# Optimization experiments

Measured on AMD Instinct MI355X. Metric: run time of the kernel, lower is better.

Reference implementation:

```python
import jax, jax.numpy as jnp
import numpy as np

B, N, M, D = 64, 512, 512, 2
BLUR, SCALING, DIAMETER, P = 0.01, 0.9, 4.0, 2


def _eps_schedule():
    # geomloss epsilon_schedule: geometric decay of temperature eps = sigma^p
    # from diameter^p down to blur^p with ratio scaling^p.
    e = np.arange(P * np.log(DIAMETER), P * np.log(BLUR), P * np.log(SCALING))
    return np.concatenate([[DIAMETER ** P], np.exp(e), [BLUR ** P]]).astype(np.float32)


def setup_inputs() -> dict:
    key = jax.random.key(0)
    k1, k2, k3, k4, k5 = jax.random.split(key, 5)
    a = jax.random.uniform(k1, (B, N), dtype=jnp.float32)
    a = a / a.sum(-1, keepdims=True)  # probability weights of measure 1
    b = jax.random.uniform(k2, (B, M), dtype=jnp.float32)
    b = b / b.sum(-1, keepdims=True)  # probability weights of measure 2
    x = jax.random.normal(k3, (B, N, D), dtype=jnp.float32)
    y = jax.random.normal(k4, (B, M, D), dtype=jnp.float32)
    w = jax.random.uniform(k5, (B,), dtype=jnp.float32)  # per-sample weights
    return {"prob1": a, "coord1": x, "prob2": b, "coord2": y, "weights": w}


def _softmin(eps, C, h):
    # softmin_eps(C, h)_i = -eps * log sum_j exp(h_j - C_ij / eps)
    # C: [B,N,M], h: [B,M] -> [B,N]
    return -eps * jax.nn.logsumexp(h[:, None, :] - C / eps, axis=2)


def reference(prob1, coord1, prob2, coord2, weights):
    a, x, b, y = prob1, coord1, prob2, coord2
    # p=2 cost: C(x,y) = |x-y|^2 / 2 (geomloss convention)
    C_xy = 0.5 * jnp.sum((x[:, :, None, :] - y[:, None, :, :]) ** 2, axis=-1)  # [B,N,M]
    C_yx = jnp.swapaxes(C_xy, 1, 2)  # [B,M,N]
    a_log = jnp.log(a)
    b_log = jnp.log(b)

    eps_arr = jnp.asarray(_eps_schedule())
    eps0 = eps_arr[0]
    # initialization at the coarsest temperature
    f = _softmin(eps0, C_xy, b_log)  # [B,N] dual potential on x
    g = _softmin(eps0, C_yx, a_log)  # [B,M] dual potential on y

    def step(carry, eps):
        f, g = carry
        ft = _softmin(eps, C_xy, b_log + g / eps)
        gt = _softmin(eps, C_yx, a_log + f / eps)
        return (0.5 * (f + ft), 0.5 * (g + gt)), None

    (f, g), _ = jax.lax.scan(step, (f, g), eps_arr)

    # geomloss runs the loop without grad and does one last extrapolation step
    f = jax.lax.stop_gradient(f)
    g = jax.lax.stop_gradient(g)
    eps_last = jnp.float32(BLUR ** P)
    f_fin = _softmin(eps_last, C_xy, b_log + g / eps_last)
    g_fin = _softmin(eps_last, C_yx, a_log + f / eps_last)

    # OT_eps(a, b) = <a, f> + <b, g>  (debias=False)
    batch_loss = jnp.sum(a * f_fin, axis=-1) + jnp.sum(b * g_fin, axis=-1)  # [B]
    return jnp.sum(batch_loss * weights)
```

## Files before the change

kernel.cpp:

```cpp
#include <hip/hip_runtime.h>
#include <cmath>

#define B_ 64
#define NP 512

constexpr float L2E  = 1.4426950408889634f;
constexpr float LN2f = 0.6931471805599453f;

struct EpsList { float e[64]; };

__device__ __forceinline__ float exp2_fast(float v) {
#if __has_builtin(__builtin_amdgcn_exp2f)
    return __builtin_amdgcn_exp2f(v);
#else
    return exp2f(v);
#endif
}
__device__ __forceinline__ float log2_fast(float v) {
#if __has_builtin(__builtin_amdgcn_logf)
    return __builtin_amdgcn_logf(v);
#else
    return log2f(v);
#endif
}

__global__ __launch_bounds__(256, 2) void sinkhorn_coop(
    const float* __restrict__ a, const float* __restrict__ x,
    const float* __restrict__ bb, const float* __restrict__ y,
    float* __restrict__ fA, float* __restrict__ gA,
    float* __restrict__ fB, float* __restrict__ gB,
    unsigned int* __restrict__ bar, float* __restrict__ part2,
    EpsList el, int n_eps)
{
    __shared__ float4 sreg[NP];
    __shared__ float4 sd[NP];
    __shared__ float s_eps[64];
    __shared__ float swred[4];

    const int bid = blockIdx.x;
    const int b   = bid >> 3;
    const int q   = bid & 7;
    const bool gside = q >= 4;
    const int rq  = q & 3;
    const int tid = threadIdx.x;
    const int oct = tid & 7;
    const int rowbase = rq * 128 + (tid >> 3) * 4;
    unsigned int* own_ctr  = bar + b * 64 + (gside ? 32 : 0);
    unsigned int* othr_ctr = bar + b * 64 + (gside ? 0 : 32);

    if (tid < 64) s_eps[tid] = el.e[tid];

    const float2* oc2   = (const float2*)(gside ? (x + b * NP * 2) : (y + b * NP * 2));
    const float*  oprob = gside ? (a + b * NP) : (bb + b * NP);
    #pragma unroll
    for (int u2 = 0; u2 < 2; ++u2) {
        int t = tid + u2 * 256;
        float2 c = oc2[t];
        sreg[t] = make_float4(c.x, c.y, fmaf(c.y, c.y, c.x * c.x),
                              L2E * logf(oprob[t]));
    }
    const float* mcoord = gside ? (y + b * NP * 2) : (x + b * NP * 2);
    const float* mprob  = gside ? (bb + b * NP)    : (a + b * NP);
    const float4 rc01 = *(const float4*)(mcoord + rowbase * 2);
    const float4 rc23 = *(const float4*)(mcoord + rowbase * 2 + 4);
    float x0[4] = {rc01.x, rc01.z, rc23.x, rc23.z};
    float x1[4] = {rc01.y, rc01.w, rc23.y, rc23.w};
    float half_n2[4];
    #pragma unroll
    for (int r = 0; r < 4; ++r) half_n2[r] = 0.5f * fmaf(x1[r], x1[r], x0[r] * x0[r]);

    float pv[4];
    const int n_pass = n_eps + 2;
    __syncthreads();

    for (int p = 0; p < n_pass; ++p) {
        const float eps = (p == 0) ? s_eps[0]
                        : (p <= n_eps ? s_eps[p - 1] : s_eps[n_eps - 1]);
        const float inv_eps = 1.0f / eps;
        const float ieL2E = inv_eps * L2E;
        const float nie   = -0.5f * ieL2E;

        float* opot = (gside ? ((p & 1) ? fA : fB)
                             : ((p & 1) ? gA : gB)) + b * NP;
        #pragma unroll
        for (int u2 = 0; u2 < 2; ++u2) {
            int t = tid + u2 * 256;
            float4 sr = sreg[t];
            float pot = (p != 0)
                ? __hip_atomic_load(opot + t, __ATOMIC_RELAXED, __HIP_MEMORY_SCOPE_AGENT)
                : 0.0f;
            float h2 = fmaf(pot, ieL2E, sr.w);
            sd[t] = make_float4(sr.x, sr.y, fmaf(nie, sr.z, h2), 0.0f);
        }
        __syncthreads();

        float x0p[4], x1p[4], m[4], s[4];
        #pragma unroll
        for (int r = 0; r < 4; ++r) {
            x0p[r] = x0[r] * ieL2E;
            x1p[r] = x1[r] * ieL2E;
            m[r] = -INFINITY;
            s[r] = 0.0f;
        }

        #pragma unroll 1
        for (int k = 0; k < 8; ++k) {
            float4 cj[8];
            #pragma unroll
            for (int u2 = 0; u2 < 8; ++u2) cj[u2] = sd[64 * k + 8 * u2 + oct];
            #pragma unroll
            for (int r = 0; r < 4; ++r) {
                float arg[8];
                #pragma unroll
                for (int u2 = 0; u2 < 8; ++u2)
                    arg[u2] = fmaf(x1p[r], cj[u2].y, fmaf(x0p[r], cj[u2].x, cj[u2].z));
                float cm = fmaxf(fmaxf(fmaxf(arg[0], arg[1]), fmaxf(arg[2], arg[3])),
                                 fmaxf(fmaxf(arg[4], arg[5]), fmaxf(arg[6], arg[7])));
                float mn = fmaxf(m[r], cm);
                s[r] *= exp2_fast(m[r] - mn);
                #pragma unroll
                for (int u2 = 0; u2 < 8; ++u2) s[r] += exp2_fast(arg[u2] - mn);
                m[r] = mn;
            }
        }

        float val[4];
        #pragma unroll
        for (int r = 0; r < 4; ++r) {
            float mr = m[r], sr = s[r];
            #pragma unroll
            for (int d = 1; d <= 4; d <<= 1) {
                float mo = __shfl_xor(mr, d);
                float so = __shfl_xor(sr, d);
                float mt = fmaxf(mr, mo);
                sr = sr * exp2_fast(mr - mt) + so * exp2_fast(mo - mt);
                mr = mt;
            }
            val[r] = fmaf(-eps * LN2f, mr + log2_fast(sr), half_n2[r]);
        }

        if (p >= 1 && p <= n_eps) {
            #pragma unroll
            for (int r = 0; r < 4; ++r) val[r] = 0.5f * (pv[r] + val[r]);
        }
        #pragma unroll
        for (int r = 0; r < 4; ++r) pv[r] = val[r];

        if (p == n_pass - 1) break;

        if (oct == 0) {
            float* dst = (gside ? ((p & 1) ? gB : gA)
                                : ((p & 1) ? fB : fA)) + b * NP + rowbase;
            #pragma unroll
            for (int r = 0; r < 4; ++r)
                __hip_atomic_store(dst + r, val[r], __ATOMIC_RELAXED,
                                   __HIP_MEMORY_SCOPE_AGENT);
        }

        __syncthreads();
        if (tid == 0) {
            __hip_atomic_fetch_add(own_ctr, 1u, __ATOMIC_RELAXED,
                                   __HIP_MEMORY_SCOPE_AGENT);
            const unsigned int target = 4u * (unsigned int)(p + 1);
            unsigned int guard = 0;
            while (__hip_atomic_load(othr_ctr, __ATOMIC_RELAXED,
                                     __HIP_MEMORY_SCOPE_AGENT) < target) {
                __builtin_amdgcn_s_sleep(1);
                if (++guard > (1u << 20)) break;
            }
        }
        __syncthreads();
    }

    float local = 0.0f;
    if (oct == 0) {
        const float4 pr = *(const float4*)(mprob + rowbase);
        local = pr.x * pv[0] + pr.y * pv[1] + pr.z * pv[2] + pr.w * pv[3];
    }
    #pragma unroll
    for (int o = 32; o > 0; o >>= 1) local += __shfl_down(local, o);
    if ((tid & 63) == 0) swred[tid >> 6] = local;
    __syncthreads();
    if (tid == 0) part2[bid] = swred[0] + swred[1] + swred[2] + swred[3];
}

__global__ void finred_k(const float* __restrict__ part2,
                         const float* __restrict__ w, float* __restrict__ out) {
    int b = threadIdx.x;
    float s = 0.0f;
    #pragma unroll
    for (int u = 0; u < 8; ++u) s += part2[b * 8 + u];
    s *= w[b];
    #pragma unroll
    for (int o = 32; o > 0; o >>= 1) s += __shfl_down(s, o);
    if (b == 0) out[0] = s;
}

extern "C" void kernel_launch(void* const* d_in, const int* in_sizes, int n_in,
                              void* d_out, int out_size, void* d_ws, size_t ws_size,
                              hipStream_t stream) {
    const float* a  = (const float*)d_in[0];
    const float* x  = (const float*)d_in[1];
    const float* bb = (const float*)d_in[2];
    const float* y  = (const float*)d_in[3];
    const float* w  = (const float*)d_in[4];
    float* out = (float*)d_out;

    unsigned char* wsb = (unsigned char*)d_ws;
    unsigned int* bar = (unsigned int*)wsb;
    float* part2 = (float*)(wsb + 64 * 64 * 4);
    float* fA = (float*)(wsb + 64 * 64 * 4 + 512 * 4);
    const int NB = B_ * NP;
    float* gA = fA + NB;
    float* fB = gA + NB;
    float* gB = fB + NB;

    EpsList el{};
    int n_eps = 0;
    {
        const double start = 2.0 * std::log(4.0);
        const double stop  = 2.0 * std::log(0.01);
        const double step  = 2.0 * std::log(0.9);
        el.e[n_eps++] = 16.0f;
        for (int k = 0;; ++k) {
            double v = start + (double)k * step;
            if (!(v > stop)) break;
            el.e[n_eps++] = (float)std::exp(v);
        }
        el.e[n_eps++] = (float)(0.01 * 0.01);
    }

    hipMemsetAsync(bar, 0, 64 * 64 * 4, stream);

    void* args[] = {
        (void*)&a, (void*)&x, (void*)&bb, (void*)&y,
        (void*)&fA, (void*)&gA, (void*)&fB, (void*)&gB,
        (void*)&bar, (void*)&part2, (void*)&el, (void*)&n_eps
    };
    hipLaunchCooperativeKernel((const void*)sinkhorn_coop,
                               dim3(B_ * 8), dim3(256), args, 0, stream);

    finred_k<<<1, 64, 0, stream>>>(part2, w, out);
}
```

Before: 527.5 us.

## Double block count per batch, pack math into float2 vectors, drop cooperative launch

```diff
diff --git a/kernel.cpp b/kernel.cpp
--- a/kernel.cpp
+++ b/kernel.cpp
@@ -6,6 +6,8 @@
 
 constexpr float L2E  = 1.4426950408889634f;
 constexpr float LN2f = 0.6931471805599453f;
+
+typedef float f32x2 __attribute__((ext_vector_type(2)));
 
 struct EpsList { float e[64]; };
 
@@ -23,8 +25,11 @@
     return log2f(v);
 #endif
 }
-
-__global__ __launch_bounds__(256, 2) void sinkhorn_coop(
+__device__ __forceinline__ f32x2 vmax2(f32x2 a, f32x2 b) {
+    return __builtin_elementwise_max(a, b);
+}
+
+__global__ __launch_bounds__(256, 4) void sinkhorn_pers(
     const float* __restrict__ a, const float* __restrict__ x,
     const float* __restrict__ bb, const float* __restrict__ y,
     float* __restrict__ fA, float* __restrict__ gA,
@@ -32,19 +37,18 @@
     unsigned int* __restrict__ bar, float* __restrict__ part2,
     EpsList el, int n_eps)
 {
-    __shared__ float4 sreg[NP];
     __shared__ float4 sd[NP];
     __shared__ float s_eps[64];
     __shared__ float swred[4];
 
     const int bid = blockIdx.x;
-    const int b   = bid >> 3;
-    const int q   = bid & 7;
-    const bool gside = q >= 4;
-    const int rq  = q & 3;
+    const int b   = bid >> 4;
+    const int q   = bid & 15;
+    const bool gside = q >= 8;
+    const int rq  = q & 7;
     const int tid = threadIdx.x;
-    const int oct = tid & 7;
-    const int rowbase = rq * 128 + (tid >> 3) * 4;
+    const int sx  = tid & 15;
+    const int rowbase = rq * 64 + (tid >> 4) * 4;
     unsigned int* own_ctr  = bar + b * 64 + (gside ? 32 : 0);
     unsigned int* othr_ctr = bar + b * 64 + (gside ? 0 : 32);
 
@@ -52,19 +56,20 @@
 
     const float2* oc2   = (const float2*)(gside ? (x + b * NP * 2) : (y + b * NP * 2));
     const float*  oprob = gside ? (a + b * NP) : (bb + b * NP);
-    #pragma unroll
-    for (int u2 = 0; u2 < 2; ++u2) {
-        int t = tid + u2 * 256;
-        float2 c = oc2[t];
-        sreg[t] = make_float4(c.x, c.y, fmaf(c.y, c.y, c.x * c.x),
-                              L2E * logf(oprob[t]));
+    float ocx[2], ocy[2], on2[2], olw[2];
+    #pragma unroll
+    for (int u = 0; u < 2; ++u) {
+        float2 c = oc2[tid + u * 256];
+        ocx[u] = c.x; ocy[u] = c.y;
+        on2[u] = fmaf(c.y, c.y, c.x * c.x);
+        olw[u] = L2E * logf(oprob[tid + u * 256]);
     }
     const float* mcoord = gside ? (y + b * NP * 2) : (x + b * NP * 2);
     const float* mprob  = gside ? (bb + b * NP)    : (a + b * NP);
     const float4 rc01 = *(const float4*)(mcoord + rowbase * 2);
     const float4 rc23 = *(const float4*)(mcoord + rowbase * 2 + 4);
-    float x0[4] = {rc01.x, rc01.z, rc23.x, rc23.z};
-    float x1[4] = {rc01.y, rc01.w, rc23.y, rc23.w};
+    const float x0[4] = {rc01.x, rc01.z, rc23.x, rc23.z};
+    const float x1[4] = {rc01.y, rc01.w, rc23.y, rc23.w};
     float half_n2[4];
     #pragma unroll
     for (int r = 0; r < 4; ++r) half_n2[r] = 0.5f * fmaf(x1[r], x1[r], x0[r] * x0[r]);
@@ -80,56 +85,69 @@
         const float ieL2E = inv_eps * L2E;
         const float nie   = -0.5f * ieL2E;
 
-        float* opot = (gside ? ((p & 1) ? fA : fB)
-                             : ((p & 1) ? gA : gB)) + b * NP;
+        {
+            float* opot = (gside ? ((p & 1) ? fA : fB)
+                                 : ((p & 1) ? gA : gB)) + b * NP;
+            #pragma unroll
+            for (int u = 0; u < 2; ++u) {
+                int t = tid + u * 256;
+                float pot = (p != 0)
+                    ? __hip_atomic_load(opot + t, __ATOMIC_RELAXED, __HIP_MEMORY_SCOPE_AGENT)
+                    : 0.0f;
+                float h2 = fmaf(pot, ieL2E, olw[u]);
+                sd[t] = make_float4(ocx[u], ocy[u], fmaf(nie, on2[u], h2), 0.0f);
+            }
+        }
+        __syncthreads();
+
+        f32x2 x0p2[2], x1p2[2], m2[2], s2[2];
         #pragma unroll
-        for (int u2 = 0; u2 < 2; ++u2) {
-            int t = tid + u2 * 256;
-            float4 sr = sreg[t];
-            float pot = (p != 0)
-                ? __hip_atomic_load(opot + t, __ATOMIC_RELAXED, __HIP_MEMORY_SCOPE_AGENT)
-                : 0.0f;
-            float h2 = fmaf(pot, ieL2E, sr.w);
-            sd[t] = make_float4(sr.x, sr.y, fmaf(nie, sr.z, h2), 0.0f);
-        }
-        __syncthreads();
-
-        float x0p[4], x1p[4], m[4], s[4];
-        #pragma unroll
-        for (int r = 0; r < 4; ++r) {
-            x0p[r] = x0[r] * ieL2E;
-            x1p[r] = x1[r] * ieL2E;
-            m[r] = -INFINITY;
-            s[r] = 0.0f;
+        for (int pr = 0; pr < 2; ++pr) {
+            x0p2[pr] = (f32x2){x0[2 * pr] * ieL2E, x0[2 * pr + 1] * ieL2E};
+            x1p2[pr] = (f32x2){x1[2 * pr] * ieL2E, x1[2 * pr + 1] * ieL2E};
+            m2[pr] = (f32x2)(-INFINITY);
+            s2[pr] = (f32x2)(0.0f);
         }
 
         #pragma unroll 1
-        for (int k = 0; k < 8; ++k) {
+        for (int k = 0; k < 4; ++k) {
             float4 cj[8];
             #pragma unroll
-            for (int u2 = 0; u2 < 8; ++u2) cj[u2] = sd[64 * k + 8 * u2 + oct];
-            #pragma unroll
-            for (int r = 0; r < 4; ++r) {
-                float arg[8];
+            for (int u = 0; u < 8; ++u) cj[u] = sd[128 * k + 16 * u + sx];
+            #pragma unroll
+            for (int pr = 0; pr < 2; ++pr) {
+                f32x2 arg[8];
                 #pragma unroll
-                for (int u2 = 0; u2 < 8; ++u2)
-                    arg[u2] = fmaf(x1p[r], cj[u2].y, fmaf(x0p[r], cj[u2].x, cj[u2].z));
-                float cm = fmaxf(fmaxf(fmaxf(arg[0], arg[1]), fmaxf(arg[2], arg[3])),
-                                 fmaxf(fmaxf(arg[4], arg[5]), fmaxf(arg[6], arg[7])));
-                float mn = fmaxf(m[r], cm);
-                s[r] *= exp2_fast(m[r] - mn);
+                for (int u = 0; u < 8; ++u) {
+                    f32x2 cx2 = cj[u].x;
+                    f32x2 cy2 = cj[u].y;
+                    f32x2 cs2 = cj[u].z;
+                    arg[u] = x1p2[pr] * cy2 + (x0p2[pr] * cx2 + cs2);
+                }
+                f32x2 cm = vmax2(vmax2(vmax2(arg[0], arg[1]), vmax2(arg[2], arg[3])),
+                                 vmax2(vmax2(arg[4], arg[5]), vmax2(arg[6], arg[7])));
+                f32x2 mn = vmax2(m2[pr], cm);
+                f32x2 dl = m2[pr] - mn;
+                f32x2 e; e.x = exp2_fast(dl.x); e.y = exp2_fast(dl.y);
+                s2[pr] *= e;
                 #pragma unroll
-                for (int u2 = 0; u2 < 8; ++u2) s[r] += exp2_fast(arg[u2] - mn);
-                m[r] = mn;
-            }
-        }
-
+                for (int u = 0; u < 8; ++u) {
+                    f32x2 t = arg[u] - mn;
+                    f32x2 et; et.x = exp2_fast(t.x); et.y = exp2_fast(t.y);
+                    s2[pr] += et;
+                }
+                m2[pr] = mn;
+            }
+        }
+
+        float m[4] = {m2[0].x, m2[0].y, m2[1].x, m2[1].y};
+        float s[4] = {s2[0].x, s2[0].y, s2[1].x, s2[1].y};
         float val[4];
         #pragma unroll
         for (int r = 0; r < 4; ++r) {
             float mr = m[r], sr = s[r];
             #pragma unroll
-            for (int d = 1; d <= 4; d <<= 1) {
+            for (int d = 1; d <= 8; d <<= 1) {
                 float mo = __shfl_xor(mr, d);
                 float so = __shfl_xor(sr, d);
                 float mt = fmaxf(mr, mo);
@@ -148,7 +166,7 @@
 
         if (p == n_pass - 1) break;
 
-        if (oct == 0) {
+        if (sx == 0) {
             float* dst = (gside ? ((p & 1) ? gB : gA)
                                 : ((p & 1) ? fB : fA)) + b * NP + rowbase;
             #pragma unroll
@@ -161,7 +179,7 @@
         if (tid == 0) {
             __hip_atomic_fetch_add(own_ctr, 1u, __ATOMIC_RELAXED,
                                    __HIP_MEMORY_SCOPE_AGENT);
-            const unsigned int target = 4u * (unsigned int)(p + 1);
+            const unsigned int target = 8u * (unsigned int)(p + 1);
             unsigned int guard = 0;
             while (__hip_atomic_load(othr_ctr, __ATOMIC_RELAXED,
                                      __HIP_MEMORY_SCOPE_AGENT) < target) {
@@ -173,7 +191,7 @@
     }
 
     float local = 0.0f;
-    if (oct == 0) {
+    if (sx == 0) {
         const float4 pr = *(const float4*)(mprob + rowbase);
         local = pr.x * pv[0] + pr.y * pv[1] + pr.z * pv[2] + pr.w * pv[3];
     }
@@ -189,7 +207,7 @@
     int b = threadIdx.x;
     float s = 0.0f;
     #pragma unroll
-    for (int u = 0; u < 8; ++u) s += part2[b * 8 + u];
+    for (int u = 0; u < 16; ++u) s += part2[b * 16 + u];
     s *= w[b];
     #pragma unroll
     for (int o = 32; o > 0; o >>= 1) s += __shfl_down(s, o);
@@ -209,7 +227,7 @@
     unsigned char* wsb = (unsigned char*)d_ws;
     unsigned int* bar = (unsigned int*)wsb;
     float* part2 = (float*)(wsb + 64 * 64 * 4);
-    float* fA = (float*)(wsb + 64 * 64 * 4 + 512 * 4);
+    float* fA = (float*)(wsb + 64 * 64 * 4 + 1024 * 4);
     const int NB = B_ * NP;
     float* gA = fA + NB;
     float* fB = gA + NB;
@@ -232,13 +250,8 @@
 
     hipMemsetAsync(bar, 0, 64 * 64 * 4, stream);
 
-    void* args[] = {
-        (void*)&a, (void*)&x, (void*)&bb, (void*)&y,
-        (void*)&fA, (void*)&gA, (void*)&fB, (void*)&gB,
-        (void*)&bar, (void*)&part2, (void*)&el, (void*)&n_eps
-    };
-    hipLaunchCooperativeKernel((const void*)sinkhorn_coop,
-                               dim3(B_ * 8), dim3(256), args, 0, stream);
+    sinkhorn_pers<<<dim3(B_ * 16), dim3(256), 0, stream>>>(
+        a, x, bb, y, fA, gA, fB, gB, bar, part2, el, n_eps);
 
     finred_k<<<1, 64, 0, stream>>>(part2, w, out);
 }
```

Result: no change. 524.9 us (-0.5%).
